# Kernel tuning notes

Measured on AMD Instinct MI355X. Metric: run time of the kernel, lower is better.

Reference implementation:

```python
import jax, jax.numpy as jnp
import numpy as np

D = 512      # embed_dim
H = 8        # num_heads
B = 32       # number of graphs
L = 512      # max graph size (padded length)
DEG = 8      # avg out-degree
NUM_GIN = 3  # StructureExtractor num_layers


def setup_inputs() -> dict:
    key = jax.random.key(0)
    ks = jax.random.split(key, 24)

    # ragged graph sizes 256..504, ptr is the CSR boundary vector
    sizes = 256 + 8 * np.arange(B)
    ptr_np = np.concatenate([[0], np.cumsum(sizes)]).astype(np.int64)
    N = int(ptr_np[-1])  # 12160 total nodes

    rng = np.random.RandomState(0)
    node_graph = np.repeat(np.arange(B), sizes)
    offs = ptr_np[node_graph]
    sz = sizes[node_graph]
    # DEG random in-graph neighbors per node
    dst = (rng.random((N, DEG)) * sz[:, None]).astype(np.int64) + offs[:, None]
    src = np.repeat(np.arange(N, dtype=np.int64), DEG)
    edge_index = jnp.asarray(np.stack([src, dst.ravel()]), dtype=jnp.int64)

    # DAG reachability mask: True = masked. Keep key 0 open so no row is fully -inf.
    md = rng.random((B, L, L)) > 0.5
    md[:, :, 0] = False
    mask_dag_ = jnp.asarray(md)

    def lin(k, fan_in, fan_out):
        return jax.random.normal(k, (fan_in, fan_out), jnp.float32) / np.sqrt(fan_in)

    inp = {
        "x": jax.random.normal(ks[0], (N, D), jnp.float32),
        "edge_index": edge_index,
        "mask_dag_": mask_dag_,
        "ptr": jnp.asarray(ptr_np),
        # GIN layers: MLP(Linear(D,D) -> ReLU -> Linear(D,D)) per layer
        "gin_w1": jnp.stack([lin(ks[1 + i], D, D) for i in range(NUM_GIN)]),
        "gin_b1": jnp.zeros((NUM_GIN, D), jnp.float32),
        "gin_w2": jnp.stack([lin(ks[4 + i], D, D) for i in range(NUM_GIN)]),
        "gin_b2": jnp.zeros((NUM_GIN, D), jnp.float32),
        "bn_gamma": jnp.ones((D,), jnp.float32),
        "bn_beta": jnp.zeros((D,), jnp.float32),
        "se_out_w": lin(ks[7], D, D),
        "se_out_b": jnp.zeros((D,), jnp.float32),
        "qk_w": lin(ks[8], D, 2 * D),
        "qk_b": jnp.zeros((2 * D,), jnp.float32),
        "v_w": lin(ks[9], D, D),
        "v_b": jnp.zeros((D,), jnp.float32),
        "out_w": lin(ks[10], D, D),
        "out_b": jnp.zeros((D,), jnp.float32),
    }
    return inp


def reference(x, edge_index, mask_dag_, ptr,
              gin_w1, gin_b1, gin_w2, gin_b2,
              bn_gamma, bn_beta, se_out_w, se_out_b,
              qk_w, qk_b, v_w, v_b, out_w, out_b):
    N = x.shape[0]
    nb = ptr.shape[0] - 1
    Lm = mask_dag_.shape[1]
    hd = D // H
    scale = hd ** -0.5

    # v = to_v(x)
    v = x @ v_w + v_b

    # StructureExtractor: 3 GIN layers (eps=0) + BatchNorm (batch stats) + Linear
    src, dst = edge_index[0], edge_index[1]
    h = x
    for i in range(NUM_GIN):
        agg = jax.ops.segment_sum(h[src], dst, num_segments=N)
        z = h + agg                                  # (1+eps)*x + sum neighbors, eps=0
        z = jax.nn.relu(z @ gin_w1[i] + gin_b1[i]) @ gin_w2[i] + gin_b2[i]
        h = jax.nn.relu(z)
    mean = h.mean(axis=0)
    var = h.var(axis=0)
    h = (h - mean) / jnp.sqrt(var + 1e-5) * bn_gamma + bn_beta
    x_struct = h @ se_out_w + se_out_b

    # qk = to_qk(x_struct).chunk(2): k = first half, q = second half (original order)
    qk = x_struct @ qk_w + qk_b
    k_flat, q_flat = jnp.split(qk, 2, axis=-1)

    # pad ragged batch to [B, L, D]
    node_ar = jnp.arange(N)
    bi = jnp.searchsorted(ptr, node_ar, side='right') - 1   # graph id per node
    pos = node_ar - ptr[bi]                                 # in-graph position
    sizes = ptr[1:] - ptr[:-1]

    def pad(t):
        return jnp.zeros((nb, Lm, t.shape[-1]), t.dtype).at[bi, pos].set(t)

    def heads(t):  # [B, L, D] -> [B, H, L, hd]
        return t.reshape(nb, Lm, H, hd).transpose(0, 2, 1, 3)

    q = heads(pad(q_flat))
    k = heads(pad(k_flat))
    vp = heads(pad(v))

    dots = jnp.einsum('bhid,bhjd->bhij', q, k) * scale
    pad_mask = jnp.arange(Lm)[None, :] >= sizes[:, None]     # True = padded key
    dots = jnp.where(pad_mask[:, None, None, :], -jnp.inf, dots)
    dots = jnp.where(mask_dag_[:, None, :, :], -jnp.inf, dots)
    attn = jax.nn.softmax(dots, axis=-1)

    out = jnp.einsum('bhij,bhjd->bhid', attn, vp)            # [B, H, L, hd]
    out = out.transpose(0, 2, 1, 3).reshape(nb, Lm, D)[bi, pos]  # unpad -> [N, D]
    return out @ out_w + out_b
```

## Files before the change

### kernel.cpp

```cpp
#include <hip/hip_runtime.h>
#include <hip/hip_bf16.h>
#include <cstdint>
#include <cstddef>

#define D 512
#define NHEAD 8
#define LMAX 512
#define NGIN 3

typedef unsigned short u16;
typedef unsigned long long u64;
typedef __attribute__((ext_vector_type(8))) short short8;
typedef __attribute__((ext_vector_type(8))) unsigned short ushort8;
typedef __attribute__((ext_vector_type(4))) unsigned short us4;
typedef __attribute__((ext_vector_type(4))) float f32x4;

static __device__ inline u16 f2bf(float f){
    union { float f; uint32_t u; } c; c.f = f;
    uint32_t r = (c.u + 0x7fffu + ((c.u >> 16) & 1u)) >> 16;
    return (u16)r;
}
static __device__ inline u16 tbf(float f){
    union { float f; uint32_t u; } c; c.f = f;
    return (u16)(c.u >> 16);
}
static __device__ inline float bf2f(u16 h){
    union { uint32_t u; float f; } c; c.u = ((uint32_t)h) << 16; return c.f;
}

#define GLOAD_LDS16(SRC, DST) \
    __builtin_amdgcn_global_load_lds( \
        (const __attribute__((address_space(1))) void*)(SRC), \
        (__attribute__((address_space(3))) void*)(DST), 16, 0, 0)

__global__ void probe_kernel(const int* __restrict__ ptr_raw,
                             const unsigned char* __restrict__ mask_raw,
                             int* __restrict__ flags){
    if (threadIdx.x == 0){
        flags[0] = (ptr_raw[1] == 0) ? 1 : 0;
        int cntOdd = 0, cnt4 = 0;
        for (int i = 1; i < 2048; i += 2) cntOdd += (mask_raw[i] != 0);
        for (int i = 4; i < 2048; i += 8) cnt4   += (mask_raw[i] != 0);
        flags[1] = (cntOdd > 64) ? 1 : ((cnt4 > 16) ? 4 : 8);
    }
}

__global__ __launch_bounds__(256) void mega_prologue(
        const float* __restrict__ v_w, const float* __restrict__ gin_w1,
        const float* __restrict__ gin_w2, const float* __restrict__ se_w,
        const float* __restrict__ out_w, const float* __restrict__ qk_w,
        u16* __restrict__ wtsh, u16* __restrict__ wtsl,
        const unsigned char* __restrict__ mask_raw, u64* __restrict__ mbits,
        const float* __restrict__ x, u16* __restrict__ Xh, u16* __restrict__ Xl,
        u16* __restrict__ sewh, u16* __restrict__ sewl,
        const int* __restrict__ ptr_raw, int* __restrict__ ptr32,
        const int* __restrict__ ei_raw, int* __restrict__ deg,
        const int* __restrict__ flags,
        int Nnodes, int E, int B, int Mn64){
    int z = blockIdx.z;
    int bid = blockIdx.y*32 + blockIdx.x;
    int tid = threadIdx.x;
    if (z <= 9){
        int Nout = (z == 9) ? 1024 : 512;
        if (z < 9 && blockIdx.x >= 16) return;
        const size_t SLOT = 262144;
        const float* W; int slot;
        switch (z){
            case 0: W = v_w; slot = 0; break;
            case 1: W = gin_w1;          slot = 1; break;
            case 2: W = gin_w2;          slot = 2; break;
            case 3: W = gin_w1 + 262144; slot = 3; break;
            case 4: W = gin_w2 + 262144; slot = 4; break;
            case 5: W = gin_w1 + 524288; slot = 5; break;
            case 6: W = gin_w2 + 524288; slot = 6; break;
            case 7: W = se_w;  slot = 7; break;
            case 8: W = out_w; slot = 10; break;
            default: W = qk_w; slot = 8; break;
        }
        u16* Wh = wtsh + SLOT*slot;
        u16* Wl = wtsl + SLOT*slot;
        __shared__ float T[32][33];
        int nb = blockIdx.x*32, kb = blockIdx.y*32;
        int ln = tid & 31, lk = tid >> 5;
        #pragma unroll
        for (int i = 0; i < 4; i++)
            T[lk + 8*i][ln] = W[(size_t)(kb + lk + 8*i)*Nout + nb + ln];
        __syncthreads();
        #pragma unroll
        for (int i = 0; i < 4; i++){
            float val = T[ln][lk + 8*i];
            u16 h = tbf(val);
            size_t idx = (size_t)(nb + lk + 8*i)*512 + kb + ln;
            Wh[idx] = h;
            Wl[idx] = tbf(val - bf2f(h));
        }
    } else if (z == 10){
        int idx = bid*256 + tid;
        if (idx >= Mn64) return;
        int w = flags[1];
        size_t ebase = (size_t)(idx >> 3) * 512 + (size_t)(idx & 7) * 64;
        u64 bits = 0;
        if (w == 1){
            const u64* p8 = (const u64*)(mask_raw + ebase);
            #pragma unroll
            for (int g = 0; g < 8; g++){
                u64 v = p8[g];
                #pragma unroll
                for (int by = 0; by < 8; by++)
                    if ((v >> (by*8)) & 0xffull) bits |= 1ull << (g*8 + by);
            }
        } else {
            for (int j = 0; j < 64; j++)
                if (mask_raw[(ebase + j) * (size_t)w]) bits |= 1ull << j;
        }
        mbits[idx] = bits;
    } else if (z == 11){
        int total4 = Nnodes*D/4;
        for (int i = bid*256 + tid; i < total4; i += 131072){
            float4 v = *(const float4*)(x + (size_t)i*4);
            float fv[4] = {v.x, v.y, v.z, v.w};
            us4 h4, l4;
            #pragma unroll
            for (int j = 0; j < 4; j++){
                u16 hh = tbf(fv[j]);
                h4[j] = hh;
                l4[j] = tbf(fv[j] - bf2f(hh));
            }
            *(us4*)(Xh + (size_t)i*4) = h4;
            *(us4*)(Xl + (size_t)i*4) = l4;
        }
    } else if (z == 12){
        int i = bid*256 + tid;
        if (i >= D*D/4) return;
        float4 v = *(const float4*)(se_w + (size_t)i*4);
        float fv[4] = {v.x, v.y, v.z, v.w};
        us4 h4, l4;
        #pragma unroll
        for (int j = 0; j < 4; j++){
            u16 hh = tbf(fv[j]);
            h4[j] = hh;
            l4[j] = tbf(fv[j] - bf2f(hh));
        }
        *(us4*)(sewh + (size_t)i*4) = h4;
        *(us4*)(sewl + (size_t)i*4) = l4;
    } else if (z == 13){
        if (bid == 0 && tid <= B)
            ptr32[tid] = flags[0] ? ptr_raw[2*tid] : ptr_raw[tid];
    } else {
        int e = bid*256 + tid;
        if (e < E){
            int d = flags[0] ? ei_raw[2*(E + e)] : ei_raw[E + e];
            if ((unsigned)d < (unsigned)Nnodes) atomicAdd(&deg[d], 1);
        }
    }
}

__global__ void scan_kernel(const int* __restrict__ deg, int* __restrict__ offs, int n){
    __shared__ int wsum[16];
    __shared__ int carry_s;
    int tid = threadIdx.x, lane = tid & 63, wv = tid >> 6;
    if (tid == 0){ carry_s = 0; offs[0] = 0; }
    __syncthreads();
    int nChunks = (n + 1023) / 1024;
    for (int ch = 0; ch < nChunks; ch++){
        int i = ch*1024 + tid;
        int val = (i < n) ? deg[i] : 0;
        int s = val;
        #pragma unroll
        for (int off = 1; off < 64; off <<= 1){
            int t = __shfl_up(s, off);
            if (lane >= off) s += t;
        }
        if (lane == 63) wsum[wv] = s;
        __syncthreads();
        if (wv == 0){
            int t = (lane < 16) ? wsum[lane] : 0;
            #pragma unroll
            for (int off = 1; off < 16; off <<= 1){
                int u = __shfl_up(t, off);
                if (lane >= off) t += u;
            }
            if (lane < 16) wsum[lane] = t;
        }
        __syncthreads();
        int wbase = wv ? wsum[wv-1] : 0;
        if (i < n) offs[i+1] = carry_s + wbase + s;
        __syncthreads();
        if (tid == 1023) carry_s += wsum[15];
        __syncthreads();
    }
}

__global__ void fill_kernel(const int* __restrict__ ei_raw, const int* __restrict__ offs,
                            int* __restrict__ cursor, int* __restrict__ in_src,
                            const int* __restrict__ flags, int E, int N){
    int e = blockIdx.x*256 + threadIdx.x;
    if (e < E){
        int d = flags[0] ? ei_raw[2*(E + e)] : ei_raw[E + e];
        if ((unsigned)d < (unsigned)N){
            int slot = atomicAdd(&cursor[d], 1);
            in_src[offs[d] + slot] = flags[0] ? ei_raw[2*e] : ei_raw[e];
        }
    }
}

__global__ __launch_bounds__(256) void gather_kernel(const u16* __restrict__ hh,
        const u16* __restrict__ hl,
        const int* __restrict__ offs, const int* __restrict__ in_src,
        u16* __restrict__ oh, u16* __restrict__ ol, int N){
    int node = blockIdx.x*2 + (threadIdx.x >> 7);
    if (node >= N) return;
    int t = threadIdx.x & 127;
    size_t rb = (size_t)node*D + t*4;
    us4 vh = *(const us4*)(hh + rb);
    us4 vl = *(const us4*)(hl + rb);
    float a[4];
    #pragma unroll
    for (int j = 0; j < 4; j++) a[j] = bf2f(vh[j]) + bf2f(vl[j]);
    int s = offs[node], e = offs[node+1];
    for (int i = s; i < e; i++){
        size_t sb = (size_t)in_src[i]*D + t*4;
        us4 nh = *(const us4*)(hh + sb);
        us4 nl = *(const us4*)(hl + sb);
        #pragma unroll
        for (int j = 0; j < 4; j++) a[j] += bf2f(nh[j]) + bf2f(nl[j]);
    }
    us4 h4, l4;
    #pragma unroll
    for (int j = 0; j < 4; j++){
        u16 hh2 = tbf(a[j]);
        h4[j] = hh2;
        l4[j] = tbf(a[j] - bf2f(hh2));
    }
    *(us4*)(oh + rb) = h4;
    *(us4*)(ol + rb) = l4;
}

__global__ __launch_bounds__(256) void fold_mega(const float* __restrict__ M1,
        const float* __restrict__ sums, const float* __restrict__ gamma,
        const float* __restrict__ beta,
        const float* __restrict__ se_b, const float* __restrict__ qk_w,
        const float* __restrict__ qk_b,
        u16* __restrict__ Wh, u16* __restrict__ Wl, float* __restrict__ bbig, int n){
    float inv_n = 1.f / (float)n;
    if (blockIdx.z == 0){
        __shared__ float T[32][33];
        int nb = blockIdx.x*32, kb = blockIdx.y*32;
        int ln = threadIdx.x & 31, lk = threadIdx.x >> 5;
        #pragma unroll
        for (int i = 0; i < 4; i++){
            int k = kb + lk + 8*i;
            float mean = sums[k] * inv_n;
            float var = sums[512+k] * inv_n - mean*mean;
            float scale = rsqrtf(var + 1e-5f) * gamma[k];
            T[lk + 8*i][ln] = M1[(size_t)k*1024 + nb + ln] * scale;
        }
        __syncthreads();
        #pragma unroll
        for (int i = 0; i < 4; i++){
            float val = T[ln][lk + 8*i];
            u16 h = tbf(val);
            size_t idx = (size_t)(nb + lk + 8*i)*512 + kb + ln;
            Wh[idx] = h;
            Wl[idx] = tbf(val - bf2f(h));
        }
    } else {
        int wv = threadIdx.x >> 6, lane = threadIdx.x & 63;
        if (wv >= 2) return;
        int nidx = (blockIdx.y*32 + blockIdx.x)*2 + wv;
        float acc = 0.f;
        for (int k = lane; k < 512; k += 64){
            float mean = sums[k] * inv_n;
            float var = sums[512+k] * inv_n - mean*mean;
            float scale = rsqrtf(var + 1e-5f) * gamma[k];
            float shift = beta[k] - mean*scale;
            acc += shift*M1[(size_t)k*1024 + nidx] + se_b[k]*qk_w[(size_t)k*1024 + nidx];
        }
        #pragma unroll
        for (int off = 32; off > 0; off >>= 1) acc += __shfl_xor(acc, off);
        if (lane == 0) bbig[nidx] = acc + qk_b[nidx];
    }
}

template<int ACT, int EPI, int TERMS>
__global__ __launch_bounds__(256) void gemm_ps(const u16* __restrict__ Ahg,
        const u16* __restrict__ Alg,
        const u16* __restrict__ Wth, const u16* __restrict__ Wtl,
        const float* __restrict__ bias,
        void* __restrict__ C0, void* __restrict__ C1, int K, int Nout){
    __shared__ __align__(16) u16 Ah[128][64];
    __shared__ __align__(16) u16 Al[TERMS == 3 ? 128 : 1][64];
    __shared__ __align__(16) u16 Bh[64][64];
    __shared__ __align__(16) u16 Bl[64][64];
    int tid = threadIdx.x;
    int gx = gridDim.x;
    int nwg = gx * gridDim.y;
    int orig = blockIdx.x + gx*blockIdx.y;
    int q8 = nwg >> 3, r8 = nwg & 7;
    int xcd = orig & 7, pos = orig >> 3;
    int wg = (xcd < r8 ? xcd*(q8+1) : r8*(q8+1) + (xcd - r8)*q8) + pos;
    int rowBase = (wg / gx) * 128, colBase = (wg % gx) * 64;
    int w = tid >> 6, l = tid & 63, lg = l >> 4, lm = l & 15;
    int wr = w >> 1, wc = w & 1;
    f32x4 acc[4][2] = {};
    const u16* Ahp = Ahg + (size_t)rowBase*K;
    const u16* Alp = (TERMS == 3) ? Alg + (size_t)rowBase*K : nullptr;
    const u16* Wph = Wth + (size_t)colBase*K;
    const u16* Wpl = Wtl + (size_t)colBase*K;
    int srowA[4], scolA[4], srowB[2], scolB[2];
    #pragma unroll
    for (int c = 0; c < 4; c++){
        int slot = c*256 + tid;
        srowA[c] = slot >> 3;
        scolA[c] = ((slot & 7) ^ (srowA[c] & 7)) * 8;
    }
    #pragma unroll
    for (int c = 0; c < 2; c++){
        int slot = c*256 + tid;
        srowB[c] = slot >> 3;
        scolB[c] = ((slot & 7) ^ (srowB[c] & 7)) * 8;
    }
    for (int k0 = 0; k0 < K; k0 += 64){
        #pragma unroll
        for (int c = 0; c < 4; c++){
            int slot = c*256 + tid;
            size_t so = (size_t)srowA[c]*K + k0 + scolA[c];
            GLOAD_LDS16(Ahp + so, &Ah[0][0] + slot*8);
            if (TERMS == 3) GLOAD_LDS16(Alp + so, &Al[0][0] + slot*8);
        }
        #pragma unroll
        for (int c = 0; c < 2; c++){
            int slot = c*256 + tid;
            size_t so = (size_t)srowB[c]*K + k0 + scolB[c];
            GLOAD_LDS16(Wph + so, &Bh[0][0] + slot*8);
            GLOAD_LDS16(Wpl + so, &Bl[0][0] + slot*8);
        }
        __syncthreads();
        #pragma unroll
        for (int ks = 0; ks < 2; ks++){
            int scg = ((ks*4 + lg) ^ (lm & 7)) * 8;
            short8 ah[4], al[4], bh[2], bl[2];
            #pragma unroll
            for (int mf = 0; mf < 4; mf++){
                ah[mf] = *(const short8*)&Ah[wr*64 + mf*16 + lm][scg];
                if (TERMS == 3) al[mf] = *(const short8*)&Al[wr*64 + mf*16 + lm][scg];
            }
            #pragma unroll
            for (int nf = 0; nf < 2; nf++){
                bh[nf] = *(const short8*)&Bh[wc*32 + nf*16 + lm][scg];
                bl[nf] = *(const short8*)&Bl[wc*32 + nf*16 + lm][scg];
            }
            __builtin_amdgcn_s_setprio(1);
            #pragma unroll
            for (int mf = 0; mf < 4; mf++)
                #pragma unroll
                for (int nf = 0; nf < 2; nf++){
                    acc[mf][nf] = __builtin_amdgcn_mfma_f32_16x16x32_bf16(ah[mf], bh[nf], acc[mf][nf], 0, 0, 0);
                    if (TERMS == 3)
                        acc[mf][nf] = __builtin_amdgcn_mfma_f32_16x16x32_bf16(al[mf], bh[nf], acc[mf][nf], 0, 0, 0);
                    acc[mf][nf] = __builtin_amdgcn_mfma_f32_16x16x32_bf16(ah[mf], bl[nf], acc[mf][nf], 0, 0, 0);
                }
            __builtin_amdgcn_s_setprio(0);
        }
        __syncthreads();
    }
    #pragma unroll
    for (int nf = 0; nf < 2; nf++){
        int col = colBase + wc*32 + nf*16 + lm;
        float bv = bias[col];
        #pragma unroll
        for (int mf = 0; mf < 4; mf++){
            int row = rowBase + wr*64 + mf*16 + lg*4;
            #pragma unroll
            for (int j = 0; j < 4; j++){
                float o = acc[mf][nf][j] + bv;
                if (ACT) o = fmaxf(o, 0.f);
                size_t idx = (size_t)(row + j)*Nout + col;
                if (EPI == 0){
                    ((float*)C0)[idx] = o;
                } else if (EPI == 1){
                    u16 hh = tbf(o);
                    ((u16*)C0)[idx] = hh;
                    ((u16*)C1)[idx] = tbf(o - bf2f(hh));
                } else {
                    ((u16*)C0)[idx] = f2bf(o);
                }
            }
        }
    }
}

__global__ __launch_bounds__(256) void bn_stats_kernel(const u16* __restrict__ Ah,
        const u16* __restrict__ Al, float* __restrict__ sums, int n){
    int c = threadIdx.x;
    int r0 = blockIdx.x*128, r1 = min(n, r0+128);
    float s0=0.f, s1=0.f, q0=0.f, q1=0.f;
    for (int r = r0; r < r1; r++){
        float v0 = bf2f(Ah[(size_t)r*D + c])       + bf2f(Al[(size_t)r*D + c]);
        float v1 = bf2f(Ah[(size_t)r*D + 256 + c]) + bf2f(Al[(size_t)r*D + 256 + c]);
        s0 += v0; q0 += v0*v0; s1 += v1; q1 += v1*v1;
    }
    atomicAdd(&sums[c], s0);
    atomicAdd(&sums[c+256], s1);
    atomicAdd(&sums[512+c], q0);
    atomicAdd(&sums[512+c+256], q1);
}

#define ATS 72
__global__ __launch_bounds__(512) void attn_mfma_kernel(const u16* __restrict__ qkH,
        const u16* __restrict__ qkL, const u16* __restrict__ vbf,
        const u64* __restrict__ maskbits,
        const int* __restrict__ ptr, u16* __restrict__ oh, int N){
    __shared__ u16 Kh[64][ATS];
    __shared__ u16 Kl[64][ATS];
    __shared__ u16 Vt[64][ATS];
    __shared__ u16 Pl[8][16][ATS];
    int b = blockIdx.z, h = blockIdx.y;
    int base = ptr[b], size = ptr[b+1] - base;
    int q0 = blockIdx.x * 128;
    if (q0 >= size) return;
    int tid = threadIdx.x, w = tid >> 6, l = tid & 63;
    int lg = l >> 4, lm = l & 15;
    short8 qh[2], ql[2];
    {
        int qrow = q0 + w*16 + lm;
        int qr = (qrow < size) ? qrow : 0;
        const u16* qph = qkH + (size_t)(base + qr)*1024 + 512 + h*64;
        const u16* qpl = qkL + (size_t)(base + qr)*1024 + 512 + h*64;
        #pragma unroll
        for (int ks = 0; ks < 2; ks++){
            short8 th = *(const short8*)(qph + ks*32 + lg*8);
            short8 tl = *(const short8*)(qpl + ks*32 + lg*8);
            if (qrow >= size){ th = short8{0,0,0,0,0,0,0,0}; tl = short8{0,0,0,0,0,0,0,0}; }
            qh[ks] = th; ql[ks] = tl;
        }
    }
    f32x4 acco[4] = {};
    float mrow[4], lrow[4];
    #pragma unroll
    for (int j = 0; j < 4; j++){ mrow[j] = -INFINITY; lrow[j] = 0.f; }
    int nt = (size + 63) >> 6;
    for (int t = 0; t < nt; t++){
        int j0 = t*64;
        __syncthreads();
        {
            int jj = tid & 63, db = (tid >> 6)*8;
            int key = j0 + jj;
            bool ok = key < size;
            size_t node = (size_t)(base + (ok ? key : 0));
            const u16* khp = qkH + node*1024 + h*64 + db;
            const u16* klp = qkL + node*1024 + h*64 + db;
            const u16* vp  = vbf + node*512  + h*64 + db;
            ushort8 z = {0,0,0,0,0,0,0,0};
            ushort8 kh0 = ok ? *(const ushort8*)(khp) : z;
            ushort8 kl0 = ok ? *(const ushort8*)(klp) : z;
            ushort8 v0  = ok ? *(const ushort8*)(vp)  : z;
            *(ushort8*)&Kh[jj][db] = kh0;
            *(ushort8*)&Kl[jj][db] = kl0;
            #pragma unroll
            for (int i = 0; i < 8; i++) Vt[db + i][jj] = v0[i];
        }
        __syncthreads();
        f32x4 sc[4] = {};
        __builtin_amdgcn_s_setprio(1);
        #pragma unroll
        for (int nf = 0; nf < 4; nf++)
            #pragma unroll
            for (int ks = 0; ks < 2; ks++){
                short8 kh = *(const short8*)&Kh[nf*16 + lm][ks*32 + lg*8];
                short8 kl = *(const short8*)&Kl[nf*16 + lm][ks*32 + lg*8];
                sc[nf] = __builtin_amdgcn_mfma_f32_16x16x32_bf16(qh[ks], kh, sc[nf], 0, 0, 0);
                sc[nf] = __builtin_amdgcn_mfma_f32_16x16x32_bf16(ql[ks], kh, sc[nf], 0, 0, 0);
                sc[nf] = __builtin_amdgcn_mfma_f32_16x16x32_bf16(qh[ks], kl, sc[nf], 0, 0, 0);
            }
        __builtin_amdgcn_s_setprio(0);
        u64 mb[4];
        #pragma unroll
        for (int j = 0; j < 4; j++)
            mb[j] = maskbits[((size_t)b*LMAX + (q0 + w*16 + lg*4 + j))*8 + t];
        float mx[4], alpha[4];
        #pragma unroll
        for (int j = 0; j < 4; j++){
            float s0 = -INFINITY;
            #pragma unroll
            for (int nf = 0; nf < 4; nf++){
                int key = j0 + nf*16 + lm;
                float s = sc[nf][j] * 0.125f;
                bool msk = (key >= size) || ((mb[j] >> (nf*16 + lm)) & 1);
                s = msk ? -INFINITY : s;
                sc[nf][j] = s;
                s0 = fmaxf(s0, s);
            }
            #pragma unroll
            for (int off = 1; off < 16; off <<= 1) s0 = fmaxf(s0, __shfl_xor(s0, off));
            mx[j] = s0;
        }
        #pragma unroll
        for (int j = 0; j < 4; j++){
            if (mx[j] == -INFINITY){ alpha[j] = 1.f; }
            else {
                float mn = fmaxf(mrow[j], mx[j]);
                alpha[j] = __expf(mrow[j] - mn);
                mrow[j] = mn;
            }
        }
        float ps[4] = {0.f, 0.f, 0.f, 0.f};
        #pragma unroll
        for (int nf = 0; nf < 4; nf++)
            #pragma unroll
            for (int j = 0; j < 4; j++){
                float p = (mx[j] == -INFINITY) ? 0.f : __expf(sc[nf][j] - mrow[j]);
                ps[j] += p;
                Pl[w][lg*4 + j][nf*16 + lm] = tbf(p);
            }
        #pragma unroll
        for (int j = 0; j < 4; j++){
            float s = ps[j];
            #pragma unroll
            for (int off = 1; off < 16; off <<= 1) s += __shfl_xor(s, off);
            lrow[j] = lrow[j]*alpha[j] + s;
        }
        #pragma unroll
        for (int df = 0; df < 4; df++)
            #pragma unroll
            for (int j = 0; j < 4; j++) acco[df][j] *= alpha[j];
        __builtin_amdgcn_s_setprio(1);
        #pragma unroll
        for (int ks = 0; ks < 2; ks++){
            short8 pf = *(const short8*)&Pl[w][lm][ks*32 + lg*8];
            #pragma unroll
            for (int df = 0; df < 4; df++){
                short8 vf = *(const short8*)&Vt[df*16 + lm][ks*32 + lg*8];
                acco[df] = __builtin_amdgcn_mfma_f32_16x16x32_bf16(pf, vf, acco[df], 0, 0, 0);
            }
        }
        __builtin_amdgcn_s_setprio(0);
    }
    #pragma unroll
    for (int j = 0; j < 4; j++){
        int r = q0 + w*16 + lg*4 + j;
        if (r < size){
            float inv = 1.f / lrow[j];
            #pragma unroll
            for (int df = 0; df < 4; df++){
                float o = acco[df][j] * inv;
                oh[(size_t)(base + r)*D + h*64 + df*16 + lm] = f2bf(o);
            }
        }
    }
}

extern "C" void kernel_launch(void* const* d_in, const int* in_sizes, int n_in,
                              void* d_out, int out_size, void* d_ws, size_t ws_size,
                              hipStream_t stream){
    const float* x        = (const float*)d_in[0];
    const int*   ei_raw   = (const int*)d_in[1];
    const unsigned char* mask_raw = (const unsigned char*)d_in[2];
    const int*   ptr_raw  = (const int*)d_in[3];
    const float* gin_w1   = (const float*)d_in[4];
    const float* gin_b1   = (const float*)d_in[5];
    const float* gin_w2   = (const float*)d_in[6];
    const float* gin_b2   = (const float*)d_in[7];
    const float* bn_gamma = (const float*)d_in[8];
    const float* bn_beta  = (const float*)d_in[9];
    const float* se_w     = (const float*)d_in[10];
    const float* se_b     = (const float*)d_in[11];
    const float* qk_w     = (const float*)d_in[12];
    const float* qk_b     = (const float*)d_in[13];
    const float* v_w      = (const float*)d_in[14];
    const float* v_b      = (const float*)d_in[15];
    const float* out_w    = (const float*)d_in[16];
    const float* out_b    = (const float*)d_in[17];

    const int N  = in_sizes[0] / D;
    const int E  = in_sizes[1] / 2;
    const int B  = in_sizes[3] - 1;
    const int Mn = in_sizes[2];

    char* ws = (char*)d_ws;
    char* p = ws;
    auto alloc = [&](size_t bytes) -> char* {
        char* q = p; p += (bytes + 255) & ~(size_t)255; return q;
    };
    size_t PLANE = (size_t)N * D * sizeof(u16);
    u16* pairX = (u16*)alloc(2*PLANE);
    u16* pairG = (u16*)alloc(2*PLANE);
    u16* pairT = (u16*)alloc(2*PLANE);
    u16* pairH = (u16*)alloc(2*PLANE);
    u16* v_bf  = (u16*)alloc(PLANE);
    u16* Xh = pairX, *Xl = pairX + (size_t)N*D;
    u16* Gh = pairG, *Gl = pairG + (size_t)N*D;
    u16* Th = pairT, *Tl = pairT + (size_t)N*D;
    u16* Hh = pairH, *Hl = pairH + (size_t)N*D;
    float* sums   = (float*)alloc(1024*sizeof(float));
    int*   flags  = (int*)alloc(16*sizeof(int));
    int*   deg    = (int*)alloc((size_t)N*sizeof(int));
    int*   offs   = (int*)alloc((size_t)(N+1)*sizeof(int));
    int*   cursor = (int*)alloc((size_t)N*sizeof(int));
    int*   in_src = (int*)alloc((size_t)E*sizeof(int));
    int*   ptr32  = (int*)alloc(64*sizeof(int));
    u64*   mbits  = (u64*)alloc((size_t)(Mn/64)*sizeof(u64));
    u16*   wtsh   = (u16*)alloc((size_t)2883584*sizeof(u16));
    u16*   wtsl   = (u16*)alloc((size_t)2883584*sizeof(u16));
    u16*   sewh   = (u16*)alloc((size_t)D*D*sizeof(u16));
    u16*   sewl   = (u16*)alloc((size_t)D*D*sizeof(u16));
    float* M1     = (float*)alloc((size_t)D*1024*sizeof(float));
    u16*   wbig_h = (u16*)alloc((size_t)1024*D*sizeof(u16));
    u16*   wbig_l = (u16*)alloc((size_t)1024*D*sizeof(u16));
    float* bbig   = (float*)alloc(1024*sizeof(float));
    float* zbias  = (float*)alloc(1024*sizeof(float));
    const size_t SLOT = 262144;
    u16 *wh_v = wtsh, *wl_v = wtsl;
    u16 *wh_g[6], *wl_g[6];
    for (int i = 0; i < 6; i++){ wh_g[i] = wtsh + SLOT*(1+i); wl_g[i] = wtsl + SLOT*(1+i); }
    u16 *wh_qk  = wtsh + SLOT*8,  *wl_qk  = wtsl + SLOT*8;
    u16 *wh_out = wtsh + SLOT*10, *wl_out = wtsl + SLOT*10;

    probe_kernel<<<1, 64, 0, stream>>>(ptr_raw, mask_raw, flags);
    hipMemsetAsync(deg, 0, (size_t)N*sizeof(int), stream);
    hipMemsetAsync(cursor, 0, (size_t)N*sizeof(int), stream);
    hipMemsetAsync(zbias, 0, 1024*sizeof(float), stream);
    hipMemsetAsync(sums, 0, 1024*sizeof(float), stream);
    mega_prologue<<<dim3(32,16,15), 256, 0, stream>>>(
        v_w, gin_w1, gin_w2, se_w, out_w, qk_w, wtsh, wtsl,
        mask_raw, mbits, x, Xh, Xl, sewh, sewl,
        ptr_raw, ptr32, ei_raw, deg, flags, N, E, B, Mn/64);
    scan_kernel<<<1, 1024, 0, stream>>>(deg, offs, N);
    fill_kernel<<<(E+255)/256, 256, 0, stream>>>(ei_raw, offs, cursor, in_src, flags, E, N);

    gemm_ps<0,0,3><<<dim3(16,4), 256, 0, stream>>>(sewh, sewl, wh_qk, wl_qk, zbias, M1, nullptr, D, 2*D);

    dim3 g512(8, N/128), g1024(16, N/128);

    gemm_ps<0,2,2><<<g512, 256, 0, stream>>>(Xh, nullptr, wh_v, wl_v, v_b, v_bf, nullptr, D, D);

    for (int i = 0; i < NGIN; i++){
        const u16* sh = (i == 0) ? Xh : Hh;
        const u16* sl = (i == 0) ? Xl : Hl;
        gather_kernel<<<(N+1)/2, 256, 0, stream>>>(sh, sl, offs, in_src, Gh, Gl, N);
        gemm_ps<1,1,3><<<g512, 256, 0, stream>>>(Gh, Gl, wh_g[2*i],   wl_g[2*i],   gin_b1 + (size_t)i*D, Th, Tl, D, D);
        gemm_ps<1,1,3><<<g512, 256, 0, stream>>>(Th, Tl, wh_g[2*i+1], wl_g[2*i+1], gin_b2 + (size_t)i*D, Hh, Hl, D, D);
    }

    bn_stats_kernel<<<(N+127)/128, 256, 0, stream>>>(Hh, Hl, sums, N);

    fold_mega<<<dim3(32,16,2), 256, 0, stream>>>(M1, sums, bn_gamma, bn_beta,
        se_b, qk_w, qk_b, wbig_h, wbig_l, bbig, N);

    gemm_ps<0,1,3><<<g1024, 256, 0, stream>>>(Hh, Hl, wbig_h, wbig_l, bbig, pairX, pairG, D, 2*D);

    attn_mfma_kernel<<<dim3(LMAX/128, NHEAD, B), 512, 0, stream>>>(pairX, pairG, v_bf, mbits, ptr32, Th, N);

    gemm_ps<0,0,2><<<g512, 256, 0, stream>>>(Th, nullptr, wh_out, wl_out, out_b, (float*)d_out, nullptr, D, D);
}
```

Before: 548.3 us.

## Fuse memsets into probe, parallelize scan, fold BN stats into GEMM, prefetch attention tiles

```diff
diff --git a/kernel.cpp b/kernel.cpp
--- a/kernel.cpp
+++ b/kernel.cpp
@@ -33,14 +33,18 @@
         (const __attribute__((address_space(1))) void*)(SRC), \
         (__attribute__((address_space(3))) void*)(DST), 16, 0, 0)
 
-__global__ void probe_kernel(const int* __restrict__ ptr_raw,
-                             const unsigned char* __restrict__ mask_raw,
-                             int* __restrict__ flags){
-    if (threadIdx.x == 0){
+__global__ __launch_bounds__(256) void probe_mega(const int* __restrict__ ptr_raw,
+        const unsigned char* __restrict__ mask_raw, int* __restrict__ flags,
+        int* __restrict__ deg, int* __restrict__ cursor,
+        float* __restrict__ sums, float* __restrict__ zbias, int N){
+    int i = blockIdx.x*256 + threadIdx.x;
+    if (i < N){ deg[i] = 0; cursor[i] = 0; }
+    if (i < 1024){ sums[i] = 0.f; zbias[i] = 0.f; }
+    if (blockIdx.x == 0 && threadIdx.x == 0){
         flags[0] = (ptr_raw[1] == 0) ? 1 : 0;
         int cntOdd = 0, cnt4 = 0;
-        for (int i = 1; i < 2048; i += 2) cntOdd += (mask_raw[i] != 0);
-        for (int i = 4; i < 2048; i += 8) cnt4   += (mask_raw[i] != 0);
+        for (int k = 1; k < 2048; k += 2) cntOdd += (mask_raw[k] != 0);
+        for (int k = 4; k < 2048; k += 8) cnt4   += (mask_raw[k] != 0);
         flags[1] = (cntOdd > 64) ? 1 : ((cnt4 > 16) ? 4 : 8);
     }
 }
@@ -155,40 +159,52 @@
     }
 }
 
-__global__ void scan_kernel(const int* __restrict__ deg, int* __restrict__ offs, int n){
+__global__ __launch_bounds__(1024) void scanA(const int* __restrict__ deg,
+        int* __restrict__ offs, int* __restrict__ totals, int n){
     __shared__ int wsum[16];
-    __shared__ int carry_s;
+    int ch = blockIdx.x;
     int tid = threadIdx.x, lane = tid & 63, wv = tid >> 6;
-    if (tid == 0){ carry_s = 0; offs[0] = 0; }
+    int i = ch*1024 + tid;
+    int val = (i < n) ? deg[i] : 0;
+    int s = val;
+    #pragma unroll
+    for (int off = 1; off < 64; off <<= 1){
+        int t = __shfl_up(s, off);
+        if (lane >= off) s += t;
+    }
+    if (lane == 63) wsum[wv] = s;
     __syncthreads();
-    int nChunks = (n + 1023) / 1024;
-    for (int ch = 0; ch < nChunks; ch++){
-        int i = ch*1024 + tid;
-        int val = (i < n) ? deg[i] : 0;
-        int s = val;
-        #pragma unroll
-        for (int off = 1; off < 64; off <<= 1){
-            int t = __shfl_up(s, off);
-            if (lane >= off) s += t;
-        }
-        if (lane == 63) wsum[wv] = s;
-        __syncthreads();
-        if (wv == 0){
-            int t = (lane < 16) ? wsum[lane] : 0;
-            #pragma unroll
-            for (int off = 1; off < 16; off <<= 1){
-                int u = __shfl_up(t, off);
-                if (lane >= off) t += u;
-            }
-            if (lane < 16) wsum[lane] = t;
-        }
-        __syncthreads();
-        int wbase = wv ? wsum[wv-1] : 0;
-        if (i < n) offs[i+1] = carry_s + wbase + s;
-        __syncthreads();
-        if (tid == 1023) carry_s += wsum[15];
-        __syncthreads();
-    }
+    if (wv == 0){
+        int t = (lane < 16) ? wsum[lane] : 0;
+        #pragma unroll
+        for (int off = 1; off < 16; off <<= 1){
+            int u = __shfl_up(t, off);
+            if (lane >= off) t += u;
+        }
+        if (lane < 16) wsum[lane] = t;
+    }
+    __syncthreads();
+    int wbase = wv ? wsum[wv-1] : 0;
+    if (i < n) offs[i+1] = wbase + s;
+    if (tid == 1023) totals[ch] = wsum[15];
+    if (ch == 0 && tid == 0) offs[0] = 0;
+}
+
+__global__ void scanB(int* __restrict__ totals, int nch){
+    int lane = threadIdx.x;
+    int v = (lane < nch) ? totals[lane] : 0;
+    int s = v;
+    #pragma unroll
+    for (int off = 1; off < 64; off <<= 1){
+        int t = __shfl_up(s, off);
+        if (lane >= off) s += t;
+    }
+    if (lane < nch) totals[lane] = s - v;
+}
+
+__global__ void scanC(int* __restrict__ offs, const int* __restrict__ totals, int n){
+    int idx = blockIdx.x*256 + threadIdx.x + 1;
+    if (idx <= n) offs[idx] += totals[(idx-1) >> 10];
 }
 
 __global__ void fill_kernel(const int* __restrict__ ei_raw, const int* __restrict__ offs,
@@ -282,12 +298,13 @@
     }
 }
 
-template<int ACT, int EPI, int TERMS>
+template<int ACT, int EPI, int TERMS, int STATS>
 __global__ __launch_bounds__(256) void gemm_ps(const u16* __restrict__ Ahg,
         const u16* __restrict__ Alg,
         const u16* __restrict__ Wth, const u16* __restrict__ Wtl,
         const float* __restrict__ bias,
-        void* __restrict__ C0, void* __restrict__ C1, int K, int Nout){
+        void* __restrict__ C0, void* __restrict__ C1,
+        float* __restrict__ stat_sums, int K, int Nout){
     __shared__ __align__(16) u16 Ah[128][64];
     __shared__ __align__(16) u16 Al[TERMS == 3 ? 128 : 1][64];
     __shared__ __align__(16) u16 Bh[64][64];
@@ -368,6 +385,7 @@
     for (int nf = 0; nf < 2; nf++){
         int col = colBase + wc*32 + nf*16 + lm;
         float bv = bias[col];
+        float ssum = 0.f, ssq = 0.f;
         #pragma unroll
         for (int mf = 0; mf < 4; mf++){
             int row = rowBase + wr*64 + mf*16 + lg*4;
@@ -375,6 +393,7 @@
             for (int j = 0; j < 4; j++){
                 float o = acc[mf][nf][j] + bv;
                 if (ACT) o = fmaxf(o, 0.f);
+                if (STATS){ ssum += o; ssq += o*o; }
                 size_t idx = (size_t)(row + j)*Nout + col;
                 if (EPI == 0){
                     ((float*)C0)[idx] = o;
@@ -387,23 +406,15 @@
                 }
             }
         }
-    }
-}
-
-__global__ __launch_bounds__(256) void bn_stats_kernel(const u16* __restrict__ Ah,
-        const u16* __restrict__ Al, float* __restrict__ sums, int n){
-    int c = threadIdx.x;
-    int r0 = blockIdx.x*128, r1 = min(n, r0+128);
-    float s0=0.f, s1=0.f, q0=0.f, q1=0.f;
-    for (int r = r0; r < r1; r++){
-        float v0 = bf2f(Ah[(size_t)r*D + c])       + bf2f(Al[(size_t)r*D + c]);
-        float v1 = bf2f(Ah[(size_t)r*D + 256 + c]) + bf2f(Al[(size_t)r*D + 256 + c]);
-        s0 += v0; q0 += v0*v0; s1 += v1; q1 += v1*v1;
-    }
-    atomicAdd(&sums[c], s0);
-    atomicAdd(&sums[c+256], s1);
-    atomicAdd(&sums[512+c], q0);
-    atomicAdd(&sums[512+c+256], q1);
+        if (STATS){
+            ssum += __shfl_xor(ssum, 16); ssum += __shfl_xor(ssum, 32);
+            ssq  += __shfl_xor(ssq, 16);  ssq  += __shfl_xor(ssq, 32);
+            if (lg == 0){
+                atomicAdd(&stat_sums[col], ssum);
+                atomicAdd(&stat_sums[512 + col], ssq);
+            }
+        }
+    }
 }
 
 #define ATS 72
@@ -421,6 +432,7 @@
     if (q0 >= size) return;
     int tid = threadIdx.x, w = tid >> 6, l = tid & 63;
     int lg = l >> 4, lm = l & 15;
+    int jj = tid & 63, db = (tid >> 6)*8;
     short8 qh[2], ql[2];
     {
         int qrow = q0 + w*16 + lm;
@@ -440,27 +452,29 @@
     #pragma unroll
     for (int j = 0; j < 4; j++){ mrow[j] = -INFINITY; lrow[j] = 0.f; }
     int nt = (size + 63) >> 6;
+    ushort8 rkh, rkl, rv;
+    auto LOADT = [&](int t, ushort8& kh0, ushort8& kl0, ushort8& v0){
+        int key = t*64 + jj;
+        bool ok = key < size;
+        size_t node = (size_t)(base + (ok ? key : 0));
+        ushort8 z = {0,0,0,0,0,0,0,0};
+        kh0 = ok ? *(const ushort8*)(qkH + node*1024 + h*64 + db) : z;
+        kl0 = ok ? *(const ushort8*)(qkL + node*1024 + h*64 + db) : z;
+        v0  = ok ? *(const ushort8*)(vbf + node*512  + h*64 + db) : z;
+    };
+    auto WRITET = [&](ushort8 kh0, ushort8 kl0, ushort8 v0){
+        *(ushort8*)&Kh[jj][db] = kh0;
+        *(ushort8*)&Kl[jj][db] = kl0;
+        #pragma unroll
+        for (int i = 0; i < 8; i++) Vt[db + i][jj] = v0[i];
+    };
+    LOADT(0, rkh, rkl, rv);
+    WRITET(rkh, rkl, rv);
+    __syncthreads();
     for (int t = 0; t < nt; t++){
         int j0 = t*64;
-        __syncthreads();
-        {
-            int jj = tid & 63, db = (tid >> 6)*8;
-            int key = j0 + jj;
-            bool ok = key < size;
-            size_t node = (size_t)(base + (ok ? key : 0));
-            const u16* khp = qkH + node*1024 + h*64 + db;
-            const u16* klp = qkL + node*1024 + h*64 + db;
-            const u16* vp  = vbf + node*512  + h*64 + db;
-            ushort8 z = {0,0,0,0,0,0,0,0};
-            ushort8 kh0 = ok ? *(const ushort8*)(khp) : z;
-            ushort8 kl0 = ok ? *(const ushort8*)(klp) : z;
-            ushort8 v0  = ok ? *(const ushort8*)(vp)  : z;
-            *(ushort8*)&Kh[jj][db] = kh0;
-            *(ushort8*)&Kl[jj][db] = kl0;
-            #pragma unroll
-            for (int i = 0; i < 8; i++) Vt[db + i][jj] = v0[i];
-        }
-        __syncthreads();
+        bool more = (t + 1) < nt;
+        if (more) LOADT(t + 1, rkh, rkl, rv);
         f32x4 sc[4] = {};
         __builtin_amdgcn_s_setprio(1);
         #pragma unroll
@@ -535,6 +549,11 @@
             }
         }
         __builtin_amdgcn_s_setprio(0);
+        if (more){
+            __syncthreads();
+            WRITET(rkh, rkl, rv);
+            __syncthreads();
+        }
     }
     #pragma unroll
     for (int j = 0; j < 4; j++){
@@ -599,6 +618,7 @@
     int*   cursor = (int*)alloc((size_t)N*sizeof(int));
     int*   in_src = (int*)alloc((size_t)E*sizeof(int));
     int*   ptr32  = (int*)alloc(64*sizeof(int));
+    int*   totals = (int*)alloc(64*sizeof(int));
     u64*   mbits  = (u64*)alloc((size_t)(Mn/64)*sizeof(u64));
     u16*   wtsh   = (u16*)alloc((size_t)2883584*sizeof(u16));
     u16*   wtsl   = (u16*)alloc((size_t)2883584*sizeof(u16));
@@ -616,40 +636,41 @@
     u16 *wh_qk  = wtsh + SLOT*8,  *wl_qk  = wtsl + SLOT*8;
     u16 *wh_out = wtsh + SLOT*10, *wl_out = wtsl + SLOT*10;
 
-    probe_kernel<<<1, 64, 0, stream>>>(ptr_raw, mask_raw, flags);
-    hipMemsetAsync(deg, 0, (size_t)N*sizeof(int), stream);
-    hipMemsetAsync(cursor, 0, (size_t)N*sizeof(int), stream);
-    hipMemsetAsync(zbias, 0, 1024*sizeof(float), stream);
-    hipMemsetAsync(sums, 0, 1024*sizeof(float), stream);
+    probe_mega<<<(N + 255)/256, 256, 0, stream>>>(ptr_raw, mask_raw, flags,
+        deg, cursor, sums, zbias, N);
     mega_prologue<<<dim3(32,16,15), 256, 0, stream>>>(
         v_w, gin_w1, gin_w2, se_w, out_w, qk_w, wtsh, wtsl,
         mask_raw, mbits, x, Xh, Xl, sewh, sewl,
         ptr_raw, ptr32, ei_raw, deg, flags, N, E, B, Mn/64);
-    scan_kernel<<<1, 1024, 0, stream>>>(deg, offs, N);
+    int nch = (N + 1023)/1024;
+    scanA<<<nch, 1024, 0, stream>>>(deg, offs, totals, N);
+    scanB<<<1, 64, 0, stream>>>(totals, nch);
+    scanC<<<(N + 255)/256, 256, 0, stream>>>(offs, totals, N);
     fill_kernel<<<(E+255)/256, 256, 0, stream>>>(ei_raw, offs, cursor, in_src, flags, E, N);
 
-    gemm_ps<0,0,3><<<dim3(16,4), 256, 0, stream>>>(sewh, sewl, wh_qk, wl_qk, zbias, M1, nullptr, D, 2*D);
+    gemm_ps<0,0,3,0><<<dim3(16,4), 256, 0, stream>>>(sewh, sewl, wh_qk, wl_qk, zbias, M1, nullptr, nullptr, D, 2*D);
 
     dim3 g512(8, N/128), g1024(16, N/128);
 
-    gemm_ps<0,2,2><<<g512, 256, 0, stream>>>(Xh, nullptr, wh_v, wl_v, v_b, v_bf, nullptr, D, D);
+    gemm_ps<0,2,2,0><<<g512, 256, 0, stream>>>(Xh, nullptr, wh_v, wl_v, v_b, v_bf, nullptr, nullptr, D, D);
 
     for (int i = 0; i < NGIN; i++){
         const u16* sh = (i == 0) ? Xh : Hh;
         const u16* sl = (i == 0) ? Xl : Hl;
         gather_kernel<<<(N+1)/2, 256, 0, stream>>>(sh, sl, offs, in_src, Gh, Gl, N);
-        gemm_ps<1,1,3><<<g512, 256, 0, stream>>>(Gh, Gl, wh_g[2*i],   wl_g[2*i],   gin_b1 + (size_t)i*D, Th, Tl, D, D);
-        gemm_ps<1,1,3><<<g512, 256, 0, stream>>>(Th, Tl, wh_g[2*i+1], wl_g[2*i+1], gin_b2 + (size_t)i*D, Hh, Hl, D, D);
-    }
-
-    bn_stats_kernel<<<(N+127)/128, 256, 0, stream>>>(Hh, Hl, sums, N);
+        gemm_ps<1,1,3,0><<<g512, 256, 0, stream>>>(Gh, Gl, wh_g[2*i], wl_g[2*i], gin_b1 + (size_t)i*D, Th, Tl, nullptr, D, D);
+        if (i == NGIN - 1)
+            gemm_ps<1,1,3,1><<<g512, 256, 0, stream>>>(Th, Tl, wh_g[2*i+1], wl_g[2*i+1], gin_b2 + (size_t)i*D, Hh, Hl, sums, D, D);
+        else
+            gemm_ps<1,1,3,0><<<g512, 256, 0, stream>>>(Th, Tl, wh_g[2*i+1], wl_g[2*i+1], gin_b2 + (size_t)i*D, Hh, Hl, nullptr, D, D);
+    }
 
     fold_mega<<<dim3(32,16,2), 256, 0, stream>>>(M1, sums, bn_gamma, bn_beta,
         se_b, qk_w, qk_b, wbig_h, wbig_l, bbig, N);
 
-    gemm_ps<0,1,3><<<g1024, 256, 0, stream>>>(Hh, Hl, wbig_h, wbig_l, bbig, pairX, pairG, D, 2*D);
+    gemm_ps<0,1,3,0><<<g1024, 256, 0, stream>>>(Hh, Hl, wbig_h, wbig_l, bbig, pairX, pairG, nullptr, D, 2*D);
 
     attn_mfma_kernel<<<dim3(LMAX/128, NHEAD, B), 512, 0, stream>>>(pairX, pairG, v_bf, mbits, ptr32, Th, N);
 
-    gemm_ps<0,0,2><<<g512, 256, 0, stream>>>(Th, nullptr, wh_out, wl_out, out_b, (float*)d_out, nullptr, D, D);
-}
+    gemm_ps<0,0,2,0><<<g512, 256, 0, stream>>>(Th, nullptr, wh_out, wl_out, out_b, (float*)d_out, nullptr, nullptr, D, D);
+}
```

Result: faster. 524.1 us (-4.4%).
